# Performance work log

Measured on AMD Instinct MI355X. Metric: run time of the kernel, lower is better.

Reference implementation:

```python
import jax, jax.numpy as jnp
import numpy as np
from jax import lax

IMG_SIZE = 512        # efficientdet-d0 input resolution
TOP_K = 256           # fixed candidate count for jit-compatible NMS
THRESHOLD = 0.01      # score threshold (init kwarg)
IOU_THRESHOLD = 0.5   # NMS IoU threshold (init kwarg)


def make_anchors():
    """Standard EfficientDet-d0 anchors: P3-P7, 3 scales x 3 ratios, xyxy."""
    strides = [8, 16, 32, 64, 128]
    scales = [2.0 ** 0, 2.0 ** (1.0 / 3.0), 2.0 ** (2.0 / 3.0)]
    ratios = [0.5, 1.0, 2.0]
    base = 4.0
    out = []
    for s in strides:
        fs = IMG_SIZE // s
        xs = (np.arange(fs, dtype=np.float32) + 0.5) * s
        cy, cx = np.meshgrid(xs, xs, indexing='ij')
        for r in ratios:
            for sc in scales:
                w = base * s * sc * np.sqrt(1.0 / r)
                h = base * s * sc * np.sqrt(r)
                a = np.stack([cx - w / 2, cy - h / 2, cx + w / 2, cy + h / 2], -1)
                out.append(a.reshape(-1, 4))
    return np.concatenate(out, 0).astype(np.float32)  # [49104, 4]


def decode_boxes(anchors, regs):
    """RetinaNet-style delta decode. anchors [A,4] xyxy, regs [B,A,4]."""
    aw = anchors[:, 2] - anchors[:, 0]
    ah = anchors[:, 3] - anchors[:, 1]
    acx = anchors[:, 0] + 0.5 * aw
    acy = anchors[:, 1] + 0.5 * ah
    dx, dy, dw, dh = regs[..., 0], regs[..., 1], regs[..., 2], regs[..., 3]
    cx = acx + dx * aw
    cy = acy + dy * ah
    w = aw * jnp.exp(jnp.clip(dw, -4.0, 4.0))
    h = ah * jnp.exp(jnp.clip(dh, -4.0, 4.0))
    boxes = jnp.stack([cx - 0.5 * w, cy - 0.5 * h, cx + 0.5 * w, cy + 0.5 * h], -1)
    return jnp.clip(boxes, 0.0, float(IMG_SIZE))  # [B,A,4]


def pairwise_iou(boxes):
    """boxes [K,4] xyxy -> iou [K,K]."""
    area = jnp.maximum(boxes[:, 2] - boxes[:, 0], 0) * jnp.maximum(boxes[:, 3] - boxes[:, 1], 0)
    lt = jnp.maximum(boxes[:, None, :2], boxes[None, :, :2])
    rb = jnp.minimum(boxes[:, None, 2:], boxes[None, :, 2:])
    wh = jnp.maximum(rb - lt, 0.0)
    inter = wh[..., 0] * wh[..., 1]
    union = area[:, None] + area[None, :] - inter
    return inter / jnp.maximum(union, 1e-8)


def nms_keep(boxes, scores):
    """Sequential NMS over score-sorted candidates. boxes [K,4], scores [K]."""
    K = boxes.shape[0]
    iou = pairwise_iou(boxes)  # [K,K]
    ar = jnp.arange(K)
    keep0 = scores > 0.0

    def body(i, keep):
        suppressed = jnp.any(keep & (iou[:, i] > IOU_THRESHOLD) & (ar < i))
        return keep.at[i].set(keep[i] & ~suppressed)

    return lax.fori_loop(0, K, body, keep0)


def setup_inputs() -> dict:
    key = jax.random.key(0)
    k1, k2 = jax.random.split(key)
    B, A, C = 8, 49104, 80
    cls_logits = jax.random.normal(k1, (B, A, C), dtype=jnp.float32) - 2.0
    box_regs = 0.2 * jax.random.normal(k2, (B, A, 4), dtype=jnp.float32)
    anchors = jnp.asarray(make_anchors())
    return {"cls_logits": cls_logits, "box_regs": box_regs, "anchors": anchors}


def reference(cls_logits, box_regs, anchors):
    probs = jax.nn.sigmoid(cls_logits)            # [B,A,C]
    scores = probs.max(-1)                        # [B,A]
    labels = probs.argmax(-1)                     # [B,A]
    boxes = decode_boxes(anchors, box_regs)       # [B,A,4]
    scores = jnp.where(scores > THRESHOLD, scores, 0.0)
    top_s, idx = lax.top_k(scores, TOP_K)         # [B,K]
    top_b = jnp.take_along_axis(boxes, idx[..., None], axis=1)   # [B,K,4]
    top_l = jnp.take_along_axis(labels, idx, axis=1)             # [B,K]
    keep = jax.vmap(nms_keep)(top_b, top_s)                      # [B,K] bool
    keep_f = keep.astype(top_b.dtype)
    dets = jnp.concatenate([top_b * keep_f[..., None], (top_s * keep_f)[..., None]], -1)  # [B,K,5]
    return dets, top_l, keep
```

## Files before the change

kernel.cpp:

```cpp
#include <hip/hip_runtime.h>
#include <stdint.h>
#include <math.h>

#define IMGF   512.0f
#define A_N    49104
#define B_N    8
#define C_N    80
#define K_N    256
#define IOU_T  0.5f
#define NBIN   4096
#define CAP    2048

__device__ __forceinline__ int bin_of(uint32_t key) {
    float s = __uint_as_float(key);
    int b = (int)(s * 4096.0f);
    return b > 4095 ? 4095 : b;
}

__global__ __launch_bounds__(256) void score_kernel(
    const float* __restrict__ logits,
    uint32_t* __restrict__ keys)
{
    const int tid  = threadIdx.x;
    const int lane = tid & 63;
    const int grp  = lane >> 2, j = lane & 3;
    const int g = blockIdx.x * 64 + (tid >> 6) * 16 + grp;

    const float4* p = (const float4*)(logits + (size_t)g * C_N);
    float4 v0 = p[j], v1 = p[j + 4], v2 = p[j + 8], v3 = p[j + 12], v4 = p[j + 16];
    float m = fmaxf(fmaxf(fmaxf(v0.x, v0.y), fmaxf(v0.z, v0.w)),
                    fmaxf(fmaxf(v1.x, v1.y), fmaxf(v1.z, v1.w)));
    m = fmaxf(m, fmaxf(fmaxf(v2.x, v2.y), fmaxf(v2.z, v2.w)));
    m = fmaxf(m, fmaxf(fmaxf(v3.x, v3.y), fmaxf(v3.z, v3.w)));
    m = fmaxf(m, fmaxf(fmaxf(v4.x, v4.y), fmaxf(v4.z, v4.w)));
    m = fmaxf(m, __shfl_xor(m, 1, 64));
    m = fmaxf(m, __shfl_xor(m, 2, 64));
    if (j == 0) {
        float s = 1.0f / (1.0f + expf(-m));
        if (!(s > 0.01f)) s = 0.0f;
        keys[g] = __float_as_uint(s);
    }
}

__global__ __launch_bounds__(1024) void select_nms_kernel(
    const uint32_t* __restrict__ keys,
    const float* __restrict__ logits,
    const float* __restrict__ regs,
    const float* __restrict__ anchors,
    float* __restrict__ out)
{
    const int b   = blockIdx.x;
    const int tid = threadIdx.x;
    const int lane = tid & 63, wv = tid >> 6;

    __shared__ uint32_t hist[NBIN];
    __shared__ int wtots[16];
    __shared__ int sh_T, sh_nc;
    __shared__ unsigned long long cand[CAP];
    __shared__ unsigned long long sorted[K_N];
    __shared__ float4 sbox[K_N];
    __shared__ float  sscore[K_N];
    __shared__ int    slab[K_N];
    __shared__ unsigned long long supr[K_N][4];
    __shared__ unsigned long long keepw[4];

    const uint32_t* kb = keys + (size_t)b * A_N;
    const uint4* kb4 = (const uint4*)kb;
    const int N4 = A_N / 4;

    for (int i = tid; i < NBIN; i += 1024) hist[i] = 0;
    if (tid == 0) sh_nc = 0;
    __syncthreads();
    for (int i = tid; i < N4; i += 1024) {
        uint4 v = kb4[i];
        atomicAdd(&hist[bin_of(v.x)], 1u);
        atomicAdd(&hist[bin_of(v.y)], 1u);
        atomicAdd(&hist[bin_of(v.z)], 1u);
        atomicAdd(&hist[bin_of(v.w)], 1u);
    }
    __syncthreads();

    const int lo = tid * 4;
    int seg = (int)hist[lo] + (int)hist[lo + 1]
            + (int)hist[lo + 2] + (int)hist[lo + 3];
    int s1 = seg;
#pragma unroll
    for (int off = 1; off < 64; off <<= 1) {
        int v = __shfl_down(s1, off, 64);
        if (lane + off < 64) s1 += v;
    }
    if (lane == 0) wtots[wv] = s1;
    __syncthreads();
    int wsuf = 0;
    for (int w = wv + 1; w < 16; ++w) wsuf += wtots[w];
    int above = wsuf + (s1 - seg);
    if (above < K_N && above + seg >= K_N) {
        int cum = above;
        for (int bin = lo + 3; bin >= lo; --bin) {
            int c = (int)hist[bin];
            if (cum + c >= K_N) { sh_T = bin; break; }
            cum += c;
        }
    }
    __syncthreads();
    const int T = sh_T;

    for (int i = tid; i < N4; i += 1024) {
        uint4 v = kb4[i];
        uint32_t ks[4] = { v.x, v.y, v.z, v.w };
#pragma unroll
        for (int q = 0; q < 4; ++q) {
            if (bin_of(ks[q]) >= T) {
                int p = atomicAdd(&sh_nc, 1);
                if (p < CAP)
                    cand[p] = ((unsigned long long)ks[q] << 32)
                            | (unsigned long long)(0xFFFFFFFFu - (uint32_t)(4 * i + q));
            }
        }
    }
    if (tid < K_N) sorted[tid] = 0ull;
    __syncthreads();
    int nc = sh_nc; if (nc > CAP) nc = CAP;

    for (int i = tid; i < nc; i += 1024) {
        unsigned long long me = cand[i];
        int r = 0;
        for (int jq = 0; jq < nc; ++jq) r += (cand[jq] > me);
        if (r < K_N) sorted[r] = me;
    }
    __syncthreads();

    if (tid < K_N) {
#pragma clang fp contract(off)
        unsigned long long cv = sorted[tid];
        uint32_t key = (uint32_t)(cv >> 32);
        uint32_t ai  = 0xFFFFFFFFu - (uint32_t)cv;
        if (ai >= (uint32_t)A_N) ai = 0;
        int a = (int)ai;
        float s = __uint_as_float(key);
        sscore[tid] = s;

        {
            const float4* lp = (const float4*)(logits + ((size_t)b * A_N + a) * C_N);
            float best = -INFINITY; int cls = 0;
#pragma unroll
            for (int k = 0; k < 20; ++k) {
                float4 w = lp[k];
                if (w.x > best) { best = w.x; cls = 4 * k + 0; }
                if (w.y > best) { best = w.y; cls = 4 * k + 1; }
                if (w.z > best) { best = w.z; cls = 4 * k + 2; }
                if (w.w > best) { best = w.w; cls = 4 * k + 3; }
            }
            slab[tid] = cls;
        }

        float ax0 = anchors[4 * a + 0], ay0 = anchors[4 * a + 1];
        float ax1 = anchors[4 * a + 2], ay1 = anchors[4 * a + 3];
        float aw = ax1 - ax0, ah = ay1 - ay0;
        float acx = ax0 + 0.5f * aw, acy = ay0 + 0.5f * ah;
        const float* r = regs + ((size_t)b * A_N + a) * 4;
        float dx = r[0], dy = r[1], dw = r[2], dh = r[3];
        float cx = acx + dx * aw;
        float cy = acy + dy * ah;
        dw = fminf(fmaxf(dw, -4.0f), 4.0f);
        dh = fminf(fmaxf(dh, -4.0f), 4.0f);
        float w = aw * expf(dw);
        float h = ah * expf(dh);
        float x0 = cx - 0.5f * w, y0 = cy - 0.5f * h;
        float x1 = cx + 0.5f * w, y1 = cy + 0.5f * h;
        x0 = fminf(fmaxf(x0, 0.0f), IMGF);
        y0 = fminf(fmaxf(y0, 0.0f), IMGF);
        x1 = fminf(fmaxf(x1, 0.0f), IMGF);
        y1 = fminf(fmaxf(y1, 0.0f), IMGF);
        sbox[tid] = make_float4(x0, y0, x1, y1);
    }
    __syncthreads();

    {
#pragma clang fp contract(off)
        const int row = tid & 255, gq = tid >> 8;
        float4 bi = sbox[row];
        float areai = fmaxf(bi.z - bi.x, 0.0f) * fmaxf(bi.w - bi.y, 0.0f);
        unsigned long long m = 0;
        const int jlo = gq * 64, jhi = jlo + 64;
        int start = row + 1 > jlo ? row + 1 : jlo;
        for (int jx = start; jx < jhi; ++jx) {
            float4 bj = sbox[jx];
            float areaj = fmaxf(bj.z - bj.x, 0.0f) * fmaxf(bj.w - bj.y, 0.0f);
            float lx = fmaxf(bi.x, bj.x), ly = fmaxf(bi.y, bj.y);
            float rx = fminf(bi.z, bj.z), ry = fminf(bi.w, bj.w);
            float iw = fmaxf(rx - lx, 0.0f), ih = fmaxf(ry - ly, 0.0f);
            float inter = iw * ih;
            float uni = areai + areaj - inter;
            float iou = inter / fmaxf(uni, 1e-8f);
            if (iou > IOU_T) m |= 1ull << (jx & 63);
        }
        supr[row][gq] = m;
    }
    if (tid < K_N) {
        unsigned long long ball = __ballot(sscore[tid] > 0.0f);
        if ((tid & 63) == 0) keepw[tid >> 6] = ball;
    }
    __syncthreads();

    if (tid == 0) {
        unsigned long long k0 = keepw[0], k1 = keepw[1], k2 = keepw[2], k3 = keepw[3];
#define NMS_CHUNK(c, kc)                                                     \
        for (int l = 0; l < 64; ++l) {                                       \
            const int i = (c) * 64 + l;                                      \
            unsigned long long w0 = supr[i][0], w1 = supr[i][1];             \
            unsigned long long w2 = supr[i][2], w3 = supr[i][3];             \
            if ((kc >> l) & 1ull) {                                          \
                k0 &= ~w0; k1 &= ~w1; k2 &= ~w2; k3 &= ~w3;                  \
            }                                                                \
        }
        NMS_CHUNK(0, k0)
        NMS_CHUNK(1, k1)
        NMS_CHUNK(2, k2)
        NMS_CHUNK(3, k3)
#undef NMS_CHUNK
        keepw[0] = k0; keepw[1] = k1; keepw[2] = k2; keepw[3] = k3;
    }
    __syncthreads();

    if (tid < K_N) {
        float keepf = ((keepw[tid >> 6] >> (tid & 63)) & 1ull) ? 1.0f : 0.0f;
        float4 bx = sbox[tid];
        float s = sscore[tid];
        float* det = out + ((size_t)b * K_N + tid) * 5;
        det[0] = bx.x * keepf;
        det[1] = bx.y * keepf;
        det[2] = bx.z * keepf;
        det[3] = bx.w * keepf;
        det[4] = s * keepf;
        out[(size_t)B_N * K_N * 5 + (size_t)b * K_N + tid] = (float)slab[tid];
        out[(size_t)B_N * K_N * 5 + (size_t)B_N * K_N + (size_t)b * K_N + tid] = keepf;
    }
}

extern "C" void kernel_launch(void* const* d_in, const int* in_sizes, int n_in,
                              void* d_out, int out_size, void* d_ws, size_t ws_size,
                              hipStream_t stream)
{
    const float* logits  = (const float*)d_in[0];
    const float* regs    = (const float*)d_in[1];
    const float* anchors = (const float*)d_in[2];
    float* out = (float*)d_out;

    uint32_t* keys = (uint32_t*)d_ws;

    const int total = B_N * A_N;
    score_kernel<<<total / 64, 256, 0, stream>>>(logits, keys);
    select_nms_kernel<<<B_N, 1024, 0, stream>>>(keys, logits, regs, anchors, out);
}
```

Measured before the change: 239.5 us.

## Compute argmax labels in score pass, cache keys in registers, vectorize rank loop

The score kernel now computes the argmax class alongside the max and writes a byte label per anchor. This removes the second read of 80 logits per selected candidate in the NMS kernel. The select kernel loads its keys into registers once and reuses them for both the histogram and candidate passes, and the rank-sort inner loop reads candidates eight at a time with 128-bit loads. Anchor and regression loads become float4, and the serial NMS loop is unrolled by four. The trade is extra register pressure from the 12 uint4 key values and one extra byte write per anchor in the score pass.

```diff
diff --git a/kernel.cpp b/kernel.cpp
--- a/kernel.cpp
+++ b/kernel.cpp
@@ -17,9 +17,17 @@
     return b > 4095 ? 4095 : b;
 }
 
+__device__ __forceinline__ void amax4(float4 v, int cbase, float& best, int& cls) {
+    if (v.x > best) { best = v.x; cls = cbase + 0; }
+    if (v.y > best) { best = v.y; cls = cbase + 1; }
+    if (v.z > best) { best = v.z; cls = cbase + 2; }
+    if (v.w > best) { best = v.w; cls = cbase + 3; }
+}
+
 __global__ __launch_bounds__(256) void score_kernel(
     const float* __restrict__ logits,
-    uint32_t* __restrict__ keys)
+    uint32_t* __restrict__ keys,
+    uint8_t* __restrict__ labels)
 {
     const int tid  = threadIdx.x;
     const int lane = tid & 63;
@@ -28,23 +36,27 @@
 
     const float4* p = (const float4*)(logits + (size_t)g * C_N);
     float4 v0 = p[j], v1 = p[j + 4], v2 = p[j + 8], v3 = p[j + 12], v4 = p[j + 16];
-    float m = fmaxf(fmaxf(fmaxf(v0.x, v0.y), fmaxf(v0.z, v0.w)),
-                    fmaxf(fmaxf(v1.x, v1.y), fmaxf(v1.z, v1.w)));
-    m = fmaxf(m, fmaxf(fmaxf(v2.x, v2.y), fmaxf(v2.z, v2.w)));
-    m = fmaxf(m, fmaxf(fmaxf(v3.x, v3.y), fmaxf(v3.z, v3.w)));
-    m = fmaxf(m, fmaxf(fmaxf(v4.x, v4.y), fmaxf(v4.z, v4.w)));
-    m = fmaxf(m, __shfl_xor(m, 1, 64));
-    m = fmaxf(m, __shfl_xor(m, 2, 64));
+    float best = -INFINITY; int cls = 0;
+    amax4(v0,      4 * j, best, cls);
+    amax4(v1, 16 + 4 * j, best, cls);
+    amax4(v2, 32 + 4 * j, best, cls);
+    amax4(v3, 48 + 4 * j, best, cls);
+    amax4(v4, 64 + 4 * j, best, cls);
+    { float mo = __shfl_xor(best, 1, 64); int co = __shfl_xor(cls, 1, 64);
+      if (mo > best || (mo == best && co < cls)) { best = mo; cls = co; } }
+    { float mo = __shfl_xor(best, 2, 64); int co = __shfl_xor(cls, 2, 64);
+      if (mo > best || (mo == best && co < cls)) { best = mo; cls = co; } }
     if (j == 0) {
-        float s = 1.0f / (1.0f + expf(-m));
+        float s = 1.0f / (1.0f + expf(-best));
         if (!(s > 0.01f)) s = 0.0f;
         keys[g] = __float_as_uint(s);
+        labels[g] = (uint8_t)cls;
     }
 }
 
 __global__ __launch_bounds__(1024) void select_nms_kernel(
     const uint32_t* __restrict__ keys,
-    const float* __restrict__ logits,
+    const uint8_t* __restrict__ labels,
     const float* __restrict__ regs,
     const float* __restrict__ anchors,
     float* __restrict__ out)
@@ -56,7 +68,7 @@
     __shared__ uint32_t hist[NBIN];
     __shared__ int wtots[16];
     __shared__ int sh_T, sh_nc;
-    __shared__ unsigned long long cand[CAP];
+    __shared__ __align__(16) unsigned long long cand[CAP];
     __shared__ unsigned long long sorted[K_N];
     __shared__ float4 sbox[K_N];
     __shared__ float  sscore[K_N];
@@ -68,15 +80,24 @@
     const uint4* kb4 = (const uint4*)kb;
     const int N4 = A_N / 4;
 
+    uint4 kv[12];
+#pragma unroll
+    for (int t = 0; t < 11; ++t) kv[t] = kb4[tid + t * 1024];
+    const bool has12 = (tid + 11 * 1024) < N4;
+    if (has12) kv[11] = kb4[tid + 11 * 1024];
+
     for (int i = tid; i < NBIN; i += 1024) hist[i] = 0;
     if (tid == 0) sh_nc = 0;
     __syncthreads();
-    for (int i = tid; i < N4; i += 1024) {
-        uint4 v = kb4[i];
-        atomicAdd(&hist[bin_of(v.x)], 1u);
-        atomicAdd(&hist[bin_of(v.y)], 1u);
-        atomicAdd(&hist[bin_of(v.z)], 1u);
-        atomicAdd(&hist[bin_of(v.w)], 1u);
+#pragma unroll
+    for (int t = 0; t < 12; ++t) {
+        if (t < 11 || has12) {
+            uint4 v = kv[t];
+            atomicAdd(&hist[bin_of(v.x)], 1u);
+            atomicAdd(&hist[bin_of(v.y)], 1u);
+            atomicAdd(&hist[bin_of(v.z)], 1u);
+            atomicAdd(&hist[bin_of(v.w)], 1u);
+        }
     }
     __syncthreads();
 
@@ -105,27 +126,43 @@
     __syncthreads();
     const int T = sh_T;
 
-    for (int i = tid; i < N4; i += 1024) {
-        uint4 v = kb4[i];
-        uint32_t ks[4] = { v.x, v.y, v.z, v.w };
-#pragma unroll
-        for (int q = 0; q < 4; ++q) {
-            if (bin_of(ks[q]) >= T) {
-                int p = atomicAdd(&sh_nc, 1);
-                if (p < CAP)
-                    cand[p] = ((unsigned long long)ks[q] << 32)
-                            | (unsigned long long)(0xFFFFFFFFu - (uint32_t)(4 * i + q));
+#pragma unroll
+    for (int t = 0; t < 12; ++t) {
+        if (t < 11 || has12) {
+            uint4 v = kv[t];
+            const int i = tid + t * 1024;
+            uint32_t ks[4] = { v.x, v.y, v.z, v.w };
+#pragma unroll
+            for (int q = 0; q < 4; ++q) {
+                if (bin_of(ks[q]) >= T) {
+                    int p = atomicAdd(&sh_nc, 1);
+                    if (p < CAP)
+                        cand[p] = ((unsigned long long)ks[q] << 32)
+                                | (unsigned long long)(0xFFFFFFFFu - (uint32_t)(4 * i + q));
+                }
             }
         }
     }
     if (tid < K_N) sorted[tid] = 0ull;
     __syncthreads();
     int nc = sh_nc; if (nc > CAP) nc = CAP;
+    const int nc8 = (nc + 7) & ~7;
+    for (int i = nc + tid; i < nc8; i += 1024) cand[i] = 0ull;
+    __syncthreads();
 
     for (int i = tid; i < nc; i += 1024) {
         unsigned long long me = cand[i];
         int r = 0;
-        for (int jq = 0; jq < nc; ++jq) r += (cand[jq] > me);
+        for (int jq = 0; jq < nc8; jq += 8) {
+            ulonglong2 c0 = *(const ulonglong2*)&cand[jq];
+            ulonglong2 c1 = *(const ulonglong2*)&cand[jq + 2];
+            ulonglong2 c2 = *(const ulonglong2*)&cand[jq + 4];
+            ulonglong2 c3 = *(const ulonglong2*)&cand[jq + 6];
+            r += (int)(c0.x > me) + (int)(c0.y > me)
+               + (int)(c1.x > me) + (int)(c1.y > me)
+               + (int)(c2.x > me) + (int)(c2.y > me)
+               + (int)(c3.x > me) + (int)(c3.y > me);
+        }
         if (r < K_N) sorted[r] = me;
     }
     __syncthreads();
@@ -139,27 +176,14 @@
         int a = (int)ai;
         float s = __uint_as_float(key);
         sscore[tid] = s;
-
-        {
-            const float4* lp = (const float4*)(logits + ((size_t)b * A_N + a) * C_N);
-            float best = -INFINITY; int cls = 0;
-#pragma unroll
-            for (int k = 0; k < 20; ++k) {
-                float4 w = lp[k];
-                if (w.x > best) { best = w.x; cls = 4 * k + 0; }
-                if (w.y > best) { best = w.y; cls = 4 * k + 1; }
-                if (w.z > best) { best = w.z; cls = 4 * k + 2; }
-                if (w.w > best) { best = w.w; cls = 4 * k + 3; }
-            }
-            slab[tid] = cls;
-        }
-
-        float ax0 = anchors[4 * a + 0], ay0 = anchors[4 * a + 1];
-        float ax1 = anchors[4 * a + 2], ay1 = anchors[4 * a + 3];
+        slab[tid] = (int)labels[(size_t)b * A_N + a];
+
+        float4 av = ((const float4*)anchors)[a];
+        float ax0 = av.x, ay0 = av.y, ax1 = av.z, ay1 = av.w;
         float aw = ax1 - ax0, ah = ay1 - ay0;
         float acx = ax0 + 0.5f * aw, acy = ay0 + 0.5f * ah;
-        const float* r = regs + ((size_t)b * A_N + a) * 4;
-        float dx = r[0], dy = r[1], dw = r[2], dh = r[3];
+        float4 rv = ((const float4*)regs)[(size_t)b * A_N + a];
+        float dx = rv.x, dy = rv.y, dw = rv.z, dh = rv.w;
         float cx = acx + dx * aw;
         float cy = acy + dy * ah;
         dw = fminf(fmaxf(dw, -4.0f), 4.0f);
@@ -205,14 +229,21 @@
 
     if (tid == 0) {
         unsigned long long k0 = keepw[0], k1 = keepw[1], k2 = keepw[2], k3 = keepw[3];
-#define NMS_CHUNK(c, kc)                                                     \
-        for (int l = 0; l < 64; ++l) {                                       \
-            const int i = (c) * 64 + l;                                      \
-            unsigned long long w0 = supr[i][0], w1 = supr[i][1];             \
-            unsigned long long w2 = supr[i][2], w3 = supr[i][3];             \
-            if ((kc >> l) & 1ull) {                                          \
-                k0 &= ~w0; k1 &= ~w1; k2 &= ~w2; k3 &= ~w3;                  \
-            }                                                                \
+#define NMS_CHUNK(c, kc)                                                       \
+        for (int l = 0; l < 64; l += 4) {                                      \
+            const int i = (c) * 64 + l;                                        \
+            unsigned long long wA0 = supr[i+0][0], wA1 = supr[i+0][1],         \
+                               wA2 = supr[i+0][2], wA3 = supr[i+0][3];         \
+            unsigned long long wB0 = supr[i+1][0], wB1 = supr[i+1][1],         \
+                               wB2 = supr[i+1][2], wB3 = supr[i+1][3];         \
+            unsigned long long wC0 = supr[i+2][0], wC1 = supr[i+2][1],         \
+                               wC2 = supr[i+2][2], wC3 = supr[i+2][3];         \
+            unsigned long long wD0 = supr[i+3][0], wD1 = supr[i+3][1],         \
+                               wD2 = supr[i+3][2], wD3 = supr[i+3][3];         \
+            if ((kc >> (l + 0)) & 1ull) { k0 &= ~wA0; k1 &= ~wA1; k2 &= ~wA2; k3 &= ~wA3; } \
+            if ((kc >> (l + 1)) & 1ull) { k0 &= ~wB0; k1 &= ~wB1; k2 &= ~wB2; k3 &= ~wB3; } \
+            if ((kc >> (l + 2)) & 1ull) { k0 &= ~wC0; k1 &= ~wC1; k2 &= ~wC2; k3 &= ~wC3; } \
+            if ((kc >> (l + 3)) & 1ull) { k0 &= ~wD0; k1 &= ~wD1; k2 &= ~wD2; k3 &= ~wD3; } \
         }
         NMS_CHUNK(0, k0)
         NMS_CHUNK(1, k1)
@@ -247,9 +278,10 @@
     const float* anchors = (const float*)d_in[2];
     float* out = (float*)d_out;
 
-    uint32_t* keys = (uint32_t*)d_ws;
+    uint32_t* keys   = (uint32_t*)d_ws;
+    uint8_t*  labels = (uint8_t*)(keys + (size_t)B_N * A_N);
 
     const int total = B_N * A_N;
-    score_kernel<<<total / 64, 256, 0, stream>>>(logits, keys);
-    select_nms_kernel<<<B_N, 1024, 0, stream>>>(keys, logits, regs, anchors, out);
-}
+    score_kernel<<<total / 64, 256, 0, stream>>>(logits, keys, labels);
+    select_nms_kernel<<<B_N, 1024, 0, stream>>>(keys, labels, regs, anchors, out);
+}
```

New measurement: 228.5 us, median of 2. 4.6% less time.
